# Kernel tuning notes

Measured on AMD Instinct MI355X. Metric: run time of the kernel, lower is better.

Reference implementation:

```python
import jax, jax.numpy as jnp
import numpy as np

N_EXPERTS = 32
TOPK = 256
DMODEL = 1024
EXPERT_SIZE = 2048
BATCH = 2
CUTOFF = 4096


def setup_inputs() -> dict:
    key = jax.random.key(0)
    k1, k2, k3, k4 = jax.random.split(key, 4)
    x = jax.random.normal(k1, (BATCH, CUTOFF, DMODEL), dtype=jnp.float32)
    # init scales ~ 1/sqrt(fan_in), mimicking get_init_weight
    gate = jax.random.normal(k2, (CUTOFF, N_EXPERTS), dtype=jnp.float32) / np.sqrt(DMODEL)
    lin1_weight = jax.random.normal(k3, (N_EXPERTS, DMODEL, EXPERT_SIZE), dtype=jnp.float32) / np.sqrt(DMODEL)
    lin2_weight = jax.random.normal(k4, (N_EXPERTS, EXPERT_SIZE, DMODEL), dtype=jnp.float32) / np.sqrt(EXPERT_SIZE)
    return {"x": x, "gate": gate, "lin1_weight": lin1_weight, "lin2_weight": lin2_weight}


def reference(x, gate, lin1_weight, lin2_weight):
    batch_size, cutoff, dmodel = x.shape
    n_experts = lin1_weight.shape[0]
    # gate scores: (batch, cutoff, n_experts) -> (n_experts, batch*cutoff)
    gate_out = jnp.einsum('bcd,ce->bce', x, gate)
    gate_out = jnp.transpose(gate_out, (2, 0, 1)).reshape(n_experts, batch_size * cutoff)
    probs = jax.nn.softmax(gate_out, axis=1)
    # top-k token selection per expert (computed but, faithfully to the original,
    # not used to gather tokens -- the original reshapes tokens contiguously)
    topk_values, topk_indices = jax.lax.top_k(probs, TOPK)
    # contiguous token -> expert grouping (as in the original reshape)
    xe = x.reshape(n_experts, TOPK, dmodel)  # requires batch*cutoff == n_experts*topk
    h = jax.nn.relu(jnp.einsum('ekd,eds->eks', xe, lin1_weight))
    out = jnp.einsum('eks,esd->ekd', h, lin2_weight)
    return out.reshape(batch_size, cutoff, dmodel)
```

## Files before the change

kernel.cpp:

```cpp
#include <hip/hip_runtime.h>
#include <hip/hip_bf16.h>

#define NE 32
#define MM 256
#define DM 1024
#define ES 2048

typedef __attribute__((ext_vector_type(8))) short short8;
typedef __attribute__((ext_vector_type(4))) float f32x4;
typedef unsigned int uint32;
typedef unsigned long long u64;
typedef unsigned short u16;

__device__ __forceinline__ uint32 cvt_pk_bf16(float a, float b) {
    uint32 r;
    asm("v_cvt_pk_bf16_f32 %0, %1, %2" : "=v"(r) : "v"(a), "v"(b));
    return r;
}
__device__ __forceinline__ u64 pack4(float a, float b, float c, float d) {
    return (u64)cvt_pk_bf16(a, b) | ((u64)cvt_pk_bf16(c, d) << 32);
}

__device__ __forceinline__ void gl_lds16(const void* g, void* l) {
    __builtin_amdgcn_global_load_lds(
        (const __attribute__((address_space(1))) uint32*)g,
        (__attribute__((address_space(3))) uint32*)l, 16, 0, 0);
}

__device__ __forceinline__ int b_off(int n, int k) {
    int X = ((n >> 2) & 7) ^ ((n & 3) << 1);
    return n * 128 + ((((k >> 3) ^ X) & 7) << 4) + (((k >> 2) & 1) << 3);
}

template<int N, int K, bool RELU, typename AT, typename CT>
__global__ __launch_bounds__(256) void ec_gemm(
    const AT* __restrict__ A,
    const float* __restrict__ B,
    CT* __restrict__ C)
{
    constexpr int BM = 128, BN = 128, BK = 64;
    constexpr int MT = MM / BM;
    constexpr int NT = N / BN;
    constexpr int NSTEP = K / BK;
    constexpr bool AF32 = (sizeof(AT) == 4);

    int bid = blockIdx.x;
    int e   = bid / (MT * NT);
    int rem = bid % (MT * NT);
    int mt  = rem / NT;
    int nt  = rem % NT;

    const AT*    Ae = A + (size_t)(e * MM + mt * BM) * K;
    const float* Be = B + (size_t)e * K * N + (size_t)nt * BN;
    CT*          Ce = C + (size_t)(e * MM + mt * BM) * N + (size_t)nt * BN;

    __shared__ char AsB[BM * BK * sizeof(AT)];
    __shared__ short Bs[BN * BK];
    char* BsB = (char*)Bs;

    const int t    = threadIdx.x;
    const int lane = t & 63;
    const int w    = t >> 6;
    const int wm   = (w >> 1) * 64;
    const int wn   = (w & 1) * 64;
    const int lr   = lane & 15;
    const int lg   = lane >> 4;

    const int bn4 = (t & 31) * 4;
    const int bkb = (t >> 5) * 4;

    f32x4  acc[4][4] = {};
    float4 br[2][4];

    auto gloadA = [&](int kt) {
        if constexpr (AF32) {
            #pragma unroll
            for (int r = 0; r < 8; ++r) {
                int reg = w * 8 + r;
                int m   = reg * 4 + (lane >> 4);
                int s   = (lane & 15) ^ (m & 7);
                const float* g = (const float*)Ae + (size_t)m * K + kt + s * 4;
                gl_lds16(g, AsB + reg * 1024);
            }
        } else {
            #pragma unroll
            for (int r = 0; r < 4; ++r) {
                int reg = w * 4 + r;
                int m   = reg * 8 + (lane >> 3);
                int s   = (lane & 7) ^ (m & 7);
                const u16* g = (const u16*)Ae + (size_t)m * K + kt + s * 8;
                gl_lds16(g, AsB + reg * 1024);
            }
        }
    };

    auto loadB = [&](int kt) {
        #pragma unroll
        for (int g = 0; g < 2; ++g) {
            int k4 = g * 32 + bkb;
            const float* Bk = Be + (size_t)(kt + k4) * N + bn4;
            br[g][0] = *(const float4*)(Bk);
            br[g][1] = *(const float4*)(Bk + N);
            br[g][2] = *(const float4*)(Bk + 2 * (size_t)N);
            br[g][3] = *(const float4*)(Bk + 3 * (size_t)N);
        }
    };
    auto writeB = [&]() {
        #pragma unroll
        for (int g = 0; g < 2; ++g) {
            int k4 = g * 32 + bkb;
            *(u64*)(BsB + b_off(bn4 + 0, k4)) = pack4(br[g][0].x, br[g][1].x, br[g][2].x, br[g][3].x);
            *(u64*)(BsB + b_off(bn4 + 1, k4)) = pack4(br[g][0].y, br[g][1].y, br[g][2].y, br[g][3].y);
            *(u64*)(BsB + b_off(bn4 + 2, k4)) = pack4(br[g][0].z, br[g][1].z, br[g][2].z, br[g][3].z);
            *(u64*)(BsB + b_off(bn4 + 3, k4)) = pack4(br[g][0].w, br[g][1].w, br[g][2].w, br[g][3].w);
        }
    };

    auto readA = [&](int i, int k) -> short8 {
        int m = wm + i * 16 + lr;
        if constexpr (AF32) {
            int s0 = (k >> 2) ^ (m & 7);
            int s1 = ((k + 4) >> 2) ^ (m & 7);
            f32x4 lo = *(const f32x4*)(AsB + m * 256 + s0 * 16);
            f32x4 hi = *(const f32x4*)(AsB + m * 256 + s1 * 16);
            union { short8 s; uint32 u[4]; } fr;
            fr.u[0] = cvt_pk_bf16(lo[0], lo[1]);
            fr.u[1] = cvt_pk_bf16(lo[2], lo[3]);
            fr.u[2] = cvt_pk_bf16(hi[0], hi[1]);
            fr.u[3] = cvt_pk_bf16(hi[2], hi[3]);
            return fr.s;
        } else {
            int s = ((k >> 3) ^ (m & 7)) & 7;
            return *(const short8*)(AsB + m * 128 + s * 16);
        }
    };

    loadB(0);
    gloadA(0);
    writeB();
    __syncthreads();

    for (int ks = 0; ks < NSTEP; ++ks) {
        const bool pf = (ks + 1 < NSTEP);
        if (pf) loadB((ks + 1) * BK);

        #pragma unroll
        for (int kk = 0; kk < 2; ++kk) {
            int k = kk * 32 + lg * 8;
            short8 af[4], bfr[4];
            #pragma unroll
            for (int i = 0; i < 4; ++i) af[i] = readA(i, k);
            #pragma unroll
            for (int j = 0; j < 4; ++j)
                bfr[j] = *(const short8*)(BsB + b_off(wn + j * 16 + lr, k));
            #pragma unroll
            for (int i = 0; i < 4; ++i)
                #pragma unroll
                for (int j = 0; j < 4; ++j)
                    acc[i][j] = __builtin_amdgcn_mfma_f32_16x16x32_bf16(af[i], bfr[j], acc[i][j], 0, 0, 0);
        }
        __syncthreads();

        if (pf) {
            gloadA((ks + 1) * BK);
            writeB();
            __syncthreads();
        }
    }

    #pragma unroll
    for (int i = 0; i < 4; ++i) {
        #pragma unroll
        for (int rr = 0; rr < 4; ++rr) {
            int row = wm + i * 16 + lg * 4 + rr;
            CT* Cp = Ce + (size_t)row * N + wn + lr;
            if constexpr (sizeof(CT) == 2) {
                #pragma unroll
                for (int jp = 0; jp < 2; ++jp) {
                    float v0 = acc[i][2 * jp + 0][rr];
                    float v1 = acc[i][2 * jp + 1][rr];
                    if constexpr (RELU) {
                        v0 = v0 > 0.0f ? v0 : 0.0f;
                        v1 = v1 > 0.0f ? v1 : 0.0f;
                    }
                    uint32 p = cvt_pk_bf16(v0, v1);
                    ((u16*)Cp)[(2 * jp + 0) * 16] = (u16)(p & 0xffffu);
                    ((u16*)Cp)[(2 * jp + 1) * 16] = (u16)(p >> 16);
                }
            } else {
                #pragma unroll
                for (int j = 0; j < 4; ++j) {
                    float v = acc[i][j][rr];
                    if constexpr (RELU) v = v > 0.0f ? v : 0.0f;
                    ((float*)Cp)[j * 16] = v;
                }
            }
        }
    }
}

extern "C" void kernel_launch(void* const* d_in, const int* in_sizes, int n_in,
                              void* d_out, int out_size, void* d_ws, size_t ws_size,
                              hipStream_t stream) {
    const float* x    = (const float*)d_in[0];
    const float* lin1 = (const float*)d_in[2];
    const float* lin2 = (const float*)d_in[3];
    float* out = (float*)d_out;
    u16* h = (u16*)d_ws;

    dim3 blk(256);
    ec_gemm<ES, DM, true,  float, u16 ><<<NE * (MM/128) * (ES/128), blk, 0, stream>>>(x, lin1, h);
    ec_gemm<DM, ES, false, u16,  float><<<NE * (MM/128) * (DM/128), blk, 0, stream>>>(h, lin2, out);
}
```

Before: 185.2 us.

## Pre-convert x to bf16 and double-buffer LDS tiles in the GEMM loop

Adds a separate kernel that converts x from fp32 to bf16 in workspace, so the first GEMM loads bf16 A tiles instead of fp32 tiles converted on every LDS read. The GEMM now keeps two LDS buffers for A and B. It issues the next tile's async A load and B register load before the MFMA work and writes B into the alternate buffer afterwards, which drops one barrier per k-step. The cost is an extra kernel launch plus a pass over x, and doubled LDS use, which may lower occupancy.

```diff
diff --git a/kernel.cpp b/kernel.cpp
--- a/kernel.cpp
+++ b/kernel.cpp
@@ -32,9 +32,19 @@
     return n * 128 + ((((k >> 3) ^ X) & 7) << 4) + (((k >> 2) & 1) << 3);
 }
 
-template<int N, int K, bool RELU, typename AT, typename CT>
+__global__ __launch_bounds__(256) void cvt_bf16(const float* __restrict__ x,
+                                                u16* __restrict__ xb, int n4) {
+    int i = blockIdx.x * blockDim.x + threadIdx.x;
+    int stride = gridDim.x * blockDim.x;
+    for (; i < n4; i += stride) {
+        float4 v = ((const float4*)x)[i];
+        ((u64*)xb)[i] = pack4(v.x, v.y, v.z, v.w);
+    }
+}
+
+template<int N, int K, bool RELU, typename CT>
 __global__ __launch_bounds__(256) void ec_gemm(
-    const AT* __restrict__ A,
+    const u16* __restrict__ A,
     const float* __restrict__ B,
     CT* __restrict__ C)
 {
@@ -42,7 +52,6 @@
     constexpr int MT = MM / BM;
     constexpr int NT = N / BN;
     constexpr int NSTEP = K / BK;
-    constexpr bool AF32 = (sizeof(AT) == 4);
 
     int bid = blockIdx.x;
     int e   = bid / (MT * NT);
@@ -50,13 +59,12 @@
     int mt  = rem / NT;
     int nt  = rem % NT;
 
-    const AT*    Ae = A + (size_t)(e * MM + mt * BM) * K;
+    const u16*   Ae = A + (size_t)(e * MM + mt * BM) * K;
     const float* Be = B + (size_t)e * K * N + (size_t)nt * BN;
     CT*          Ce = C + (size_t)(e * MM + mt * BM) * N + (size_t)nt * BN;
 
-    __shared__ char AsB[BM * BK * sizeof(AT)];
-    __shared__ short Bs[BN * BK];
-    char* BsB = (char*)Bs;
+    __shared__ char AsB[2][BM * BK * 2];
+    __shared__ char BsB[2][BN * BK * 2];
 
     const int t    = threadIdx.x;
     const int lane = t & 63;
@@ -72,28 +80,16 @@
     f32x4  acc[4][4] = {};
     float4 br[2][4];
 
-    auto gloadA = [&](int kt) {
-        if constexpr (AF32) {
-            #pragma unroll
-            for (int r = 0; r < 8; ++r) {
-                int reg = w * 8 + r;
-                int m   = reg * 4 + (lane >> 4);
-                int s   = (lane & 15) ^ (m & 7);
-                const float* g = (const float*)Ae + (size_t)m * K + kt + s * 4;
-                gl_lds16(g, AsB + reg * 1024);
-            }
-        } else {
-            #pragma unroll
-            for (int r = 0; r < 4; ++r) {
-                int reg = w * 4 + r;
-                int m   = reg * 8 + (lane >> 3);
-                int s   = (lane & 7) ^ (m & 7);
-                const u16* g = (const u16*)Ae + (size_t)m * K + kt + s * 8;
-                gl_lds16(g, AsB + reg * 1024);
-            }
+    auto gloadA = [&](int kt, int buf) {
+        #pragma unroll
+        for (int r = 0; r < 4; ++r) {
+            int reg = w * 4 + r;
+            int m   = reg * 8 + (lane >> 3);
+            int s   = (lane & 7) ^ (m & 7);
+            const u16* g = Ae + (size_t)m * K + kt + s * 8;
+            gl_lds16(g, AsB[buf] + reg * 1024);
         }
     };
-
     auto loadB = [&](int kt) {
         #pragma unroll
         for (int g = 0; g < 2; ++g) {
@@ -105,67 +101,49 @@
             br[g][3] = *(const float4*)(Bk + 3 * (size_t)N);
         }
     };
-    auto writeB = [&]() {
+    auto writeB = [&](int buf) {
         #pragma unroll
         for (int g = 0; g < 2; ++g) {
             int k4 = g * 32 + bkb;
-            *(u64*)(BsB + b_off(bn4 + 0, k4)) = pack4(br[g][0].x, br[g][1].x, br[g][2].x, br[g][3].x);
-            *(u64*)(BsB + b_off(bn4 + 1, k4)) = pack4(br[g][0].y, br[g][1].y, br[g][2].y, br[g][3].y);
-            *(u64*)(BsB + b_off(bn4 + 2, k4)) = pack4(br[g][0].z, br[g][1].z, br[g][2].z, br[g][3].z);
-            *(u64*)(BsB + b_off(bn4 + 3, k4)) = pack4(br[g][0].w, br[g][1].w, br[g][2].w, br[g][3].w);
+            *(u64*)(BsB[buf] + b_off(bn4 + 0, k4)) = pack4(br[g][0].x, br[g][1].x, br[g][2].x, br[g][3].x);
+            *(u64*)(BsB[buf] + b_off(bn4 + 1, k4)) = pack4(br[g][0].y, br[g][1].y, br[g][2].y, br[g][3].y);
+            *(u64*)(BsB[buf] + b_off(bn4 + 2, k4)) = pack4(br[g][0].z, br[g][1].z, br[g][2].z, br[g][3].z);
+            *(u64*)(BsB[buf] + b_off(bn4 + 3, k4)) = pack4(br[g][0].w, br[g][1].w, br[g][2].w, br[g][3].w);
         }
     };
-
-    auto readA = [&](int i, int k) -> short8 {
+    auto readA = [&](int i, int k, int buf) -> short8 {
         int m = wm + i * 16 + lr;
-        if constexpr (AF32) {
-            int s0 = (k >> 2) ^ (m & 7);
-            int s1 = ((k + 4) >> 2) ^ (m & 7);
-            f32x4 lo = *(const f32x4*)(AsB + m * 256 + s0 * 16);
-            f32x4 hi = *(const f32x4*)(AsB + m * 256 + s1 * 16);
-            union { short8 s; uint32 u[4]; } fr;
-            fr.u[0] = cvt_pk_bf16(lo[0], lo[1]);
-            fr.u[1] = cvt_pk_bf16(lo[2], lo[3]);
-            fr.u[2] = cvt_pk_bf16(hi[0], hi[1]);
-            fr.u[3] = cvt_pk_bf16(hi[2], hi[3]);
-            return fr.s;
-        } else {
-            int s = ((k >> 3) ^ (m & 7)) & 7;
-            return *(const short8*)(AsB + m * 128 + s * 16);
-        }
+        int s = ((k >> 3) ^ (m & 7)) & 7;
+        return *(const short8*)(AsB[buf] + m * 128 + s * 16);
     };
 
     loadB(0);
-    gloadA(0);
-    writeB();
+    gloadA(0, 0);
+    writeB(0);
     __syncthreads();
 
     for (int ks = 0; ks < NSTEP; ++ks) {
+        const int  c  = ks & 1;
         const bool pf = (ks + 1 < NSTEP);
-        if (pf) loadB((ks + 1) * BK);
+        if (pf) { gloadA((ks + 1) * BK, c ^ 1); loadB((ks + 1) * BK); }
 
         #pragma unroll
         for (int kk = 0; kk < 2; ++kk) {
             int k = kk * 32 + lg * 8;
             short8 af[4], bfr[4];
             #pragma unroll
-            for (int i = 0; i < 4; ++i) af[i] = readA(i, k);
+            for (int i = 0; i < 4; ++i) af[i] = readA(i, k, c);
             #pragma unroll
             for (int j = 0; j < 4; ++j)
-                bfr[j] = *(const short8*)(BsB + b_off(wn + j * 16 + lr, k));
+                bfr[j] = *(const short8*)(BsB[c] + b_off(wn + j * 16 + lr, k));
             #pragma unroll
             for (int i = 0; i < 4; ++i)
                 #pragma unroll
                 for (int j = 0; j < 4; ++j)
                     acc[i][j] = __builtin_amdgcn_mfma_f32_16x16x32_bf16(af[i], bfr[j], acc[i][j], 0, 0, 0);
         }
+        if (pf) writeB(c ^ 1);
         __syncthreads();
-
-        if (pf) {
-            gloadA((ks + 1) * BK);
-            writeB();
-            __syncthreads();
-        }
     }
 
     #pragma unroll
@@ -206,9 +184,12 @@
     const float* lin1 = (const float*)d_in[2];
     const float* lin2 = (const float*)d_in[3];
     float* out = (float*)d_out;
-    u16* h = (u16*)d_ws;
+
+    u16* h  = (u16*)d_ws;
+    u16* xb = (u16*)((char*)d_ws + (size_t)36 * 1024 * 1024);
 
     dim3 blk(256);
-    ec_gemm<ES, DM, true,  float, u16 ><<<NE * (MM/128) * (ES/128), blk, 0, stream>>>(x, lin1, h);
-    ec_gemm<DM, ES, false, u16,  float><<<NE * (MM/128) * (DM/128), blk, 0, stream>>>(h, lin2, out);
+    cvt_bf16<<<2048, blk, 0, stream>>>(x, xb, NE * MM * DM / 4);
+    ec_gemm<ES, DM, true,  u16  ><<<NE * (MM/128) * (ES/128), blk, 0, stream>>>(xb, lin1, h);
+    ec_gemm<DM, ES, false, float><<<NE * (MM/128) * (DM/128), blk, 0, stream>>>(h, lin2, out);
 }
```

Result: slower. 190.5 us (+2.8%).
